# Kernel tuning notes

Hardware: AMD Instinct MI355X
Metric: run time of the kernel (lower is better)

Reference implementation:

```python
import jax, jax.numpy as jnp
import numpy as np

N, E, NS, NB = 25000, 400000, 4, 8
S0, V0 = 64, 32            # input: 64x0e + 32x1o
MS, MV = 96, 96            # message irreps: 96x0e + 96x1o
OS, OV = 128, 32           # post-linear_down/skip: (64+64)x0e + 32x1o
NIRR = S0 + V0             # node_feats.irreps.num_irreps = 96
AVG_NEIGH = 16.0
Y1 = float(np.sqrt(3.0 / (4.0 * np.pi)))  # integral-normalized l=1 SH coeff


def setup_inputs() -> dict:
    key = jax.random.key(0)
    k = jax.random.split(key, 15)
    return {
        'node_feats': jax.random.normal(k[0], (N, S0 + 3 * V0), jnp.float32),
        'vectors': jax.random.normal(k[1], (E, 3), jnp.float32),
        'rbf': jax.random.uniform(k[2], (E, NB), jnp.float32),
        'species': jax.random.randint(k[3], (N,), 0, NS, jnp.int32),
        'senders': jax.random.randint(k[4], (E,), 0, N, jnp.int32),
        'receivers': jax.random.randint(k[5], (E,), 0, N, jnp.int32),
        'W_up_s': jax.random.normal(k[6], (S0, S0), jnp.float32),
        'W_up_v': jax.random.normal(k[7], (V0, V0), jnp.float32),
        'W_mlp1': jax.random.normal(k[8], (NB, 64), jnp.float32),
        'W_mlp2': jax.random.normal(k[9], (64, 64), jnp.float32),
        'W_mlp3': jax.random.normal(k[10], (64, MS + MV), jnp.float32),
        'W_down_s': jax.random.normal(k[11], (MS, OS), jnp.float32),
        'W_down_v': jax.random.normal(k[12], (MV, OV), jnp.float32),
        'W_skip_s': jax.random.normal(k[13], (NS, S0, OS), jnp.float32),
        'W_skip_v': jax.random.normal(k[14], (NS, V0, OV), jnp.float32),
    }


def reference(node_feats, vectors, rbf, species, senders, receivers,
              W_up_s, W_up_v, W_mlp1, W_mlp2, W_mlp3,
              W_down_s, W_down_v, W_skip_s, W_skip_v):
    n = node_feats.shape[0]
    s = node_feats[:, :S0]                      # [N, 64]   0e
    v = node_feats[:, S0:].reshape(n, V0, 3)    # [N, 32,3] 1o

    # linear_up (per-irrep linear, 1/sqrt(fan_in) path normalization), then gather
    s_up = (s @ W_up_s) * (1.0 / jnp.sqrt(S0))
    v_up = jnp.einsum('nci,cd->ndi', v, W_up_v) * (1.0 / jnp.sqrt(V0))
    s_e = s_up[senders]                         # [E, 64]
    v_e = v_up[senders]                         # [E, 32, 3]

    # spherical harmonics l=1, normalize=True, 'integral' normalization
    y = Y1 * vectors / (jnp.linalg.norm(vectors, axis=-1, keepdims=True) + 1e-12)

    # tensor products filtered to output irreps + 0e
    tp_v = s_e[:, :, None] * y[:, None, :]                       # 0e x 1o -> 1o [E,64,3]
    tp_s = jnp.einsum('eci,ei->ec', v_e, y) * (1.0 / jnp.sqrt(3.0))  # 1o x 1o -> 0e [E,32]
    msg_s = jnp.concatenate([s_e, tp_s], axis=1)                 # [E, 96]
    msg_v = jnp.concatenate([v_e, tp_v], axis=1)                 # [E, 96, 3]

    # radial MLP -> per-edge, per-irrep mixing weights
    h = jax.nn.silu(rbf @ W_mlp1 * (1.0 / jnp.sqrt(NB)))
    h = jax.nn.silu(h @ W_mlp2 * (1.0 / 8.0))
    mix = h @ W_mlp3 * (1.0 / 8.0)                               # [E, 192]

    inv = 1.0 / NIRR
    msg_s = msg_s * mix[:, :MS] * inv
    msg_v = msg_v * (mix[:, MS:] * inv)[:, :, None]

    # scatter-sum to receivers, then normalize by sqrt(avg_num_neighbors)
    agg_s = jax.ops.segment_sum(msg_s, receivers, num_segments=n) / jnp.sqrt(AVG_NEIGH)
    agg_v = jax.ops.segment_sum(msg_v, receivers, num_segments=n) / jnp.sqrt(AVG_NEIGH)

    # linear_down to 128x0e + 32x1o
    out_s = agg_s @ W_down_s * (1.0 / jnp.sqrt(MS))
    out_v = jnp.einsum('nci,cd->ndi', agg_v, W_down_v) * (1.0 / jnp.sqrt(MV))

    # species-indexed skip connection (indexed linear)
    skip_s = jnp.einsum('nc,ncd->nd', s, W_skip_s[species]) * (1.0 / jnp.sqrt(S0))
    skip_v = jnp.einsum('nci,ncd->ndi', v, W_skip_v[species]) * (1.0 / jnp.sqrt(V0))

    f_s = out_s + skip_s                                         # [N, 128]
    f_v = out_v + skip_v                                         # [N, 32, 3]

    # equivariant gate: first 96 scalars activated, last 32 scalars gate the vectors
    act_s = jax.nn.silu(f_s[:, :OS - OV])
    gates = jax.nn.silu(f_s[:, OS - OV:])
    gated_v = f_v * gates[:, :, None]
    return jnp.concatenate([act_s, gated_v.reshape(n, OV * 3)], axis=1)  # [N, 192]
```

## Files before the change

### kernel.cpp

```cpp
#include <hip/hip_runtime.h>
#include <hip/hip_bf16.h>
#include <hip/hip_fp16.h>
#include <hip/hip_fp8.h>

#define NN 25000
#define EE 400000

#define SC_UP_S 0.125f
#define SC_UP_V 0.17677669529663689f
#define Y1C 0.48860251190291992f
#define SC_MLP1 0.35355339059327373f
#define SC_MLP2 0.125f
#define SC3 0.0013020833333333333f
#define INV_SQRT3 0.57735026918962584f
#define SC_DOWN 0.025515518153991442f
#define SC_SKIP_S 0.125f
#define SC_SKIP_V 0.17677669529663689f

typedef __attribute__((ext_vector_type(8))) short short8;
typedef __attribute__((ext_vector_type(4))) float f32x4;

__device__ __forceinline__ float silu(float x) {
  return __fdividef(x, 1.f + __expf(-x));
}
__device__ __forceinline__ unsigned short f2bf(float f) {
  unsigned u = __float_as_uint(f);
  unsigned r = u + 0x7FFF + ((u >> 16) & 1);
  return (unsigned short)(r >> 16);
}
__device__ __forceinline__ float bf2f(unsigned short s) {
  return __uint_as_float(((unsigned)s) << 16);
}
__device__ __forceinline__ unsigned packbf(float lo, float hi) {
  return ((unsigned)f2bf(hi) << 16) | (unsigned)f2bf(lo);
}
__device__ __forceinline__ unsigned char f2fp8(float x) {
  __hip_fp8_e4m3 v(x);
  return (unsigned char)v.__x;
}
__device__ __forceinline__ float fp82f(unsigned b) {
  __hip_fp8_e4m3 t;
  t.__x = (__hip_fp8_storage_t)b;
  return (float)t;
}

#define W_W1P 0
#define W_W2P 1024
#define W_W3B 3072
#define W_WDS 9216
#define W_WDV 15360
#define W_SUP 16896
#define W_VUP (W_SUP + NN * 64)
#define W_DEG (W_VUP + NN * 96)
#define W_PRE (W_DEG + NN)
#define W_CUR (W_PRE + NN + 8)
#define W_SRT (W_CUR + NN)
#define W_EDN (W_SRT + EE * 2)
#define W_END (W_EDN + EE * 56)

__global__ __launch_bounds__(256) void transpose_weights(
    const float* __restrict__ W1, const float* __restrict__ W2,
    const float* __restrict__ W3, const float* __restrict__ Wds,
    const float* __restrict__ Wdv, float* __restrict__ ws) {
  int t = blockIdx.x * 256 + threadIdx.x;
  int stride = gridDim.x * 256;
  unsigned short* W1p = (unsigned short*)(ws + W_W1P);
  unsigned short* W2p = (unsigned short*)(ws + W_W2P);
  unsigned short* W3b = (unsigned short*)(ws + W_W3B);
  unsigned short* Wdsb = (unsigned short*)(ws + W_WDS);
  unsigned short* Wdvb = (unsigned short*)(ws + W_WDV);
  for (int i = t; i < 2048; i += stride) {
    int c = i >> 5, k = i & 31;
    W1p[i] = (k < 8) ? f2bf(W1[k * 64 + c] * SC_MLP1) : (unsigned short)0;
  }
  for (int i = t; i < 4096; i += stride) {
    int c = i >> 6, k = i & 63;
    W2p[i] = f2bf(W2[k * 64 + c] * SC_MLP2);
  }
  for (int i = t; i < 12288; i += stride) {
    int c = i >> 6, k = i & 63;
    float sc = (c >= 64 && c < 96) ? (SC3 * INV_SQRT3) : SC3;
    W3b[i] = f2bf(W3[k * 192 + c] * sc);
  }
  for (int i = t; i < 12288; i += stride) {
    int o = i / 96, k = i - 96 * o;
    Wdsb[i] = f2bf(Wds[k * 128 + o] * SC_DOWN);
  }
  for (int i = t; i < 3072; i += stride) {
    int o = i / 96, k = i - 96 * o;
    Wdvb[i] = f2bf(Wdv[k * 32 + o] * SC_DOWN);
  }
}

__global__ __launch_bounds__(256) void up_kernel(
    const float* __restrict__ nf, const float* __restrict__ Wus,
    const float* __restrict__ Wuv, float* __restrict__ s_up,
    float* __restrict__ v_up) {
  int n = blockIdx.x;
  int t = threadIdx.x;
  __shared__ float sv[160];
  if (t < 160) sv[t] = nf[n * 160 + t];
  __syncthreads();
  if (t < 64) {
    float a = 0.f;
#pragma unroll
    for (int k = 0; k < 64; k++) a += sv[k] * Wus[k * 64 + t];
    s_up[n * 64 + t] = a * SC_UP_S;
  } else if (t < 160) {
    int j = t - 64;
    int c = j / 3, i = j - 3 * c;
    float a = 0.f;
#pragma unroll
    for (int k = 0; k < 32; k++) a += sv[64 + k * 3 + i] * Wuv[k * 32 + c];
    v_up[n * 96 + j] = a * SC_UP_V;
  }
}

__global__ __launch_bounds__(256) void count_deg(
    const int* __restrict__ receivers, int* __restrict__ deg) {
  int e = blockIdx.x * 256 + threadIdx.x;
  if (e < EE) atomicAdd(&deg[receivers[e]], 1);
}

__global__ __launch_bounds__(1024) void scan_kernel(
    const int* __restrict__ deg, int* __restrict__ prefix) {
  __shared__ int waveSums[16];
  __shared__ int sCarry;
  int t = threadIdx.x;
  int lane = t & 63, wv = t >> 6;
  if (t == 0) sCarry = 0;
  __syncthreads();
  for (int base = 0; base < NN; base += 1024) {
    int i = base + t;
    int x = (i < NN) ? deg[i] : 0;
    int v = x;
#pragma unroll
    for (int d = 1; d < 64; d <<= 1) {
      int u = __shfl_up(v, d, 64);
      if (lane >= d) v += u;
    }
    if (lane == 63) waveSums[wv] = v;
    __syncthreads();
    if (wv == 0 && lane < 16) {
      int s = waveSums[lane];
#pragma unroll
      for (int d = 1; d < 16; d <<= 1) {
        int u = __shfl_up(s, d, 64);
        if (lane >= d) s += u;
      }
      waveSums[lane] = s;
    }
    __syncthreads();
    int waveOff = (wv == 0) ? 0 : waveSums[wv - 1];
    int incl = v + waveOff + sCarry;
    if (i < NN) prefix[i] = incl - x;
    __syncthreads();
    if (t == 1023) sCarry = incl;
    __syncthreads();
  }
  if (t == 0) prefix[NN] = sCarry;
}

__global__ __launch_bounds__(256) void copy_cursor(
    const int* __restrict__ prefix, int* __restrict__ cursor) {
  int i = blockIdx.x * 256 + threadIdx.x;
  if (i < NN) cursor[i] = prefix[i];
}

__global__ __launch_bounds__(256) void scatter_kernel(
    const int* __restrict__ senders, const int* __restrict__ receivers,
    int* __restrict__ cursor, int2* __restrict__ sorted) {
  int e = blockIdx.x * 256 + threadIdx.x;
  if (e < EE) {
    int r = receivers[e];
    int pos = atomicAdd(&cursor[r], 1);
    sorted[pos] = make_int2(e, senders[e]);
  }
}

__global__ __launch_bounds__(256, 4) void edge_down2(
    const float* __restrict__ rbf, const float* __restrict__ vectors,
    const int2* __restrict__ sorted,
    const unsigned short* __restrict__ W1p,
    const unsigned short* __restrict__ W2p,
    const unsigned short* __restrict__ W3b,
    const unsigned short* __restrict__ Wdsb,
    const unsigned short* __restrict__ Wdvb,
    const float* __restrict__ s_up, const float* __restrict__ v_up,
    unsigned char* __restrict__ edown) {
  __shared__ unsigned short sH[64 * 72];
  __shared__ unsigned short sMix[64 * 200];
  __shared__ float4 sY[64];

  int t = threadIdx.x;
  int pbase = blockIdx.x * 64;
  int lane = t & 63;
  int wv = t >> 6;
  int rl = lane & 15;
  int kgrp = lane >> 4;
  int arow = 16 * wv + rl;
  int crow = 16 * wv + kgrp * 4;

  if (t < 64) {
    int2 es = sorted[pbase + t];
    float vx = vectors[(size_t)es.x * 3 + 0];
    float vy = vectors[(size_t)es.x * 3 + 1];
    float vz = vectors[(size_t)es.x * 3 + 2];
    float nrm = sqrtf(vx * vx + vy * vy + vz * vz) + 1e-12f;
    float ysc = Y1C / nrm;
    sY[t] = make_float4(vx * ysc, vy * ysc, vz * ysc, __int_as_float(es.y));
  }

  union S8 { short8 v; unsigned u[4]; };

  S8 a1;
  a1.u[0] = a1.u[1] = a1.u[2] = a1.u[3] = 0u;
  if (kgrp == 0) {
    int eid = sorted[pbase + arow].x;
    float4 ra = *(const float4*)(rbf + (size_t)eid * 8);
    float4 rb = *(const float4*)(rbf + (size_t)eid * 8 + 4);
    a1.u[0] = packbf(ra.x, ra.y);
    a1.u[1] = packbf(ra.z, ra.w);
    a1.u[2] = packbf(rb.x, rb.y);
    a1.u[3] = packbf(rb.z, rb.w);
  }
#pragma unroll
  for (int ct = 0; ct < 4; ct++) {
    short8 b = *(const short8*)&W1p[(ct * 16 + rl) * 32 + kgrp * 8];
    f32x4 acc = {0.f, 0.f, 0.f, 0.f};
    acc = __builtin_amdgcn_mfma_f32_16x16x32_bf16(a1.v, b, acc, 0, 0, 0);
#pragma unroll
    for (int rr = 0; rr < 4; rr++)
      sH[(crow + rr) * 72 + ct * 16 + rl] = f2bf(silu(acc[rr]));
  }

  {
    short8 a20 = *(const short8*)&sH[arow * 72 + kgrp * 8];
    short8 a21 = *(const short8*)&sH[arow * 72 + 32 + kgrp * 8];
#pragma unroll
    for (int ct = 0; ct < 4; ct++) {
      const unsigned short* wb = &W2p[(ct * 16 + rl) * 64];
      short8 b0 = *(const short8*)&wb[kgrp * 8];
      short8 b1 = *(const short8*)&wb[32 + kgrp * 8];
      f32x4 acc = {0.f, 0.f, 0.f, 0.f};
      acc = __builtin_amdgcn_mfma_f32_16x16x32_bf16(a20, b0, acc, 0, 0, 0);
      acc = __builtin_amdgcn_mfma_f32_16x16x32_bf16(a21, b1, acc, 0, 0, 0);
#pragma unroll
      for (int rr = 0; rr < 4; rr++)
        sH[(crow + rr) * 72 + ct * 16 + rl] = f2bf(silu(acc[rr]));
    }
  }

  {
    short8 a30 = *(const short8*)&sH[arow * 72 + kgrp * 8];
    short8 a31 = *(const short8*)&sH[arow * 72 + 32 + kgrp * 8];
#pragma unroll
    for (int nt = 0; nt < 12; nt++) {
      int cc = nt * 16 + rl;
      const unsigned short* wb = &W3b[cc * 64];
      short8 b0 = *(const short8*)&wb[kgrp * 8];
      short8 b1 = *(const short8*)&wb[32 + kgrp * 8];
      f32x4 acc = {0.f, 0.f, 0.f, 0.f};
      acc = __builtin_amdgcn_mfma_f32_16x16x32_bf16(a30, b0, acc, 0, 0, 0);
      acc = __builtin_amdgcn_mfma_f32_16x16x32_bf16(a31, b1, acc, 0, 0, 0);
#pragma unroll
      for (int rr = 0; rr < 4; rr++)
        sMix[(crow + rr) * 200 + cc] = f2bf(acc[rr]);
    }
  }
  __syncthreads();

  float4 yv = sY[arow];
  int snd = __float_as_int(yv.w);
  const float* se = s_up + (size_t)snd * 64;
  const float* ve = v_up + (size_t)snd * 96;
  float se1[8], se2[8], vvv[24];
  *(float4*)&se1[0] = *(const float4*)(se + kgrp * 8);
  *(float4*)&se1[4] = *(const float4*)(se + kgrp * 8 + 4);
  *(float4*)&se2[0] = *(const float4*)(se + 32 + kgrp * 8);
  *(float4*)&se2[4] = *(const float4*)(se + 32 + kgrp * 8 + 4);
#pragma unroll
  for (int j = 0; j < 6; j++)
    *(float4*)&vvv[4 * j] = *(const float4*)(ve + 24 * kgrp + 4 * j);

  const unsigned short* mrow = &sMix[arow * 200];
  S8 as0, as1, as2, mvp1, mvp2, mvp3;
  {
    short8 m = *(const short8*)&mrow[kgrp * 8];
#pragma unroll
    for (int q = 0; q < 4; q++)
      as0.u[q] = packbf(se1[2 * q] * bf2f((unsigned short)m[2 * q]),
                        se1[2 * q + 1] * bf2f((unsigned short)m[2 * q + 1]));
  }
  {
    short8 m = *(const short8*)&mrow[32 + kgrp * 8];
#pragma unroll
    for (int q = 0; q < 4; q++)
      as1.u[q] = packbf(se2[2 * q] * bf2f((unsigned short)m[2 * q]),
                        se2[2 * q + 1] * bf2f((unsigned short)m[2 * q + 1]));
  }
  {
    short8 m = *(const short8*)&mrow[64 + kgrp * 8];
#pragma unroll
    for (int q = 0; q < 4; q++) {
      float d0 = vvv[6 * q] * yv.x + vvv[6 * q + 1] * yv.y + vvv[6 * q + 2] * yv.z;
      float d1 = vvv[6 * q + 3] * yv.x + vvv[6 * q + 4] * yv.y + vvv[6 * q + 5] * yv.z;
      as2.u[q] = packbf(d0 * bf2f((unsigned short)m[2 * q]),
                        d1 * bf2f((unsigned short)m[2 * q + 1]));
    }
  }
  mvp1.v = *(const short8*)&mrow[96 + kgrp * 8];
  mvp2.v = *(const short8*)&mrow[128 + kgrp * 8];
  mvp3.v = *(const short8*)&mrow[160 + kgrp * 8];
  __syncthreads();

  unsigned char* edL = (unsigned char*)sMix;
#pragma unroll
  for (int ot = 0; ot < 8; ot++) {
    int col = ot * 16 + rl;
    const unsigned short* wb = &Wdsb[col * 96];
    short8 b0 = *(const short8*)&wb[kgrp * 8];
    short8 b1 = *(const short8*)&wb[32 + kgrp * 8];
    short8 b2 = *(const short8*)&wb[64 + kgrp * 8];
    f32x4 acc = {0.f, 0.f, 0.f, 0.f};
    acc = __builtin_amdgcn_mfma_f32_16x16x32_bf16(as0.v, b0, acc, 0, 0, 0);
    acc = __builtin_amdgcn_mfma_f32_16x16x32_bf16(as1.v, b1, acc, 0, 0, 0);
    acc = __builtin_amdgcn_mfma_f32_16x16x32_bf16(as2.v, b2, acc, 0, 0, 0);
#pragma unroll
    for (int rr = 0; rr < 4; rr++)
      edL[(crow + rr) * 232 + col] = f2fp8(acc[rr]);
  }
  float yarr[3] = {yv.x, yv.y, yv.z};
#pragma unroll
  for (int i = 0; i < 3; i++) {
    S8 av0, av1, av2;
#pragma unroll
    for (int q = 0; q < 4; q++) {
      av0.u[q] = packbf(
          vvv[3 * (2 * q) + i] * bf2f((unsigned short)mvp1.v[2 * q]),
          vvv[3 * (2 * q + 1) + i] * bf2f((unsigned short)mvp1.v[2 * q + 1]));
      av1.u[q] = packbf(
          se1[2 * q] * yarr[i] * bf2f((unsigned short)mvp2.v[2 * q]),
          se1[2 * q + 1] * yarr[i] * bf2f((unsigned short)mvp2.v[2 * q + 1]));
      av2.u[q] = packbf(
          se2[2 * q] * yarr[i] * bf2f((unsigned short)mvp3.v[2 * q]),
          se2[2 * q + 1] * yarr[i] * bf2f((unsigned short)mvp3.v[2 * q + 1]));
    }
#pragma unroll
    for (int ot = 0; ot < 2; ot++) {
      int o = ot * 16 + rl;
      const unsigned short* wb = &Wdvb[o * 96];
      short8 b0 = *(const short8*)&wb[kgrp * 8];
      short8 b1 = *(const short8*)&wb[32 + kgrp * 8];
      short8 b2 = *(const short8*)&wb[64 + kgrp * 8];
      f32x4 acc = {0.f, 0.f, 0.f, 0.f};
      acc = __builtin_amdgcn_mfma_f32_16x16x32_bf16(av0.v, b0, acc, 0, 0, 0);
      acc = __builtin_amdgcn_mfma_f32_16x16x32_bf16(av1.v, b1, acc, 0, 0, 0);
      acc = __builtin_amdgcn_mfma_f32_16x16x32_bf16(av2.v, b2, acc, 0, 0, 0);
#pragma unroll
      for (int rr = 0; rr < 4; rr++)
        edL[(crow + rr) * 232 + 128 + o * 3 + i] = f2fp8(acc[rr]);
    }
  }
  __syncthreads();

  {
    int row = t >> 2, q = t & 3;
    const unsigned* src = (const unsigned*)(edL + row * 232 + q * 56);
    unsigned* dst = (unsigned*)(edown + (size_t)(pbase + row) * 224 + q * 56);
#pragma unroll
    for (int j = 0; j < 14; j++) dst[j] = src[j];
  }
}

__global__ __launch_bounds__(256) void gather_out3(
    const float* __restrict__ nf, const int* __restrict__ species,
    const int* __restrict__ prefix, const unsigned* __restrict__ edw,
    const float* __restrict__ Wss, const float* __restrict__ Wsv,
    float* __restrict__ out) {
  int n = blockIdx.x;
  int t = threadIdx.x;
  __shared__ float sNF[160];
  __shared__ float4 sPart[4][56];
  __shared__ float sEd[224];
  __shared__ float sF[224];
  if (t < 160) sNF[t] = nf[(size_t)n * 160 + t];
  int beg = prefix[n], end = prefix[n + 1];
  if (t < 224) {
    int u = t % 56, rg = t / 56;
    float a0 = 0.f, a1 = 0.f, a2 = 0.f, a3 = 0.f;
    for (int s = beg + rg; s < end; s += 4) {
      unsigned v = edw[(size_t)s * 56 + u];
      a0 += fp82f(v & 0xFF);
      a1 += fp82f((v >> 8) & 0xFF);
      a2 += fp82f((v >> 16) & 0xFF);
      a3 += fp82f(v >> 24);
    }
    sPart[rg][u] = make_float4(a0, a1, a2, a3);
  }
  __syncthreads();
  if (t < 56) {
    float4 a = sPart[0][t], b = sPart[1][t], c = sPart[2][t], d = sPart[3][t];
    sEd[4 * t + 0] = a.x + b.x + c.x + d.x;
    sEd[4 * t + 1] = a.y + b.y + c.y + d.y;
    sEd[4 * t + 2] = a.z + b.z + c.z + d.z;
    sEd[4 * t + 3] = a.w + b.w + c.w + d.w;
  }
  __syncthreads();
  int spec = species[n];
  if (t < 128) {
    const float* wsk = Wss + (size_t)spec * 64 * 128;
    float b = 0.f;
#pragma unroll
    for (int k = 0; k < 64; k++) b += sNF[k] * wsk[k * 128 + t];
    sF[t] = sEd[t] + b * SC_SKIP_S;
  } else if (t < 224) {
    int j = t - 128;
    int c = j / 3, i = j - 3 * c;
    const float* wsk = Wsv + (size_t)spec * 32 * 32;
    float b = 0.f;
#pragma unroll
    for (int k = 0; k < 32; k++) b += sNF[64 + k * 3 + i] * wsk[k * 32 + c];
    sF[t] = sEd[t] + b * SC_SKIP_V;
  }
  __syncthreads();
  if (t < 96) {
    out[(size_t)n * 192 + t] = silu(sF[t]);
  } else if (t < 192) {
    int j = t - 96;
    int c = j / 3;
    out[(size_t)n * 192 + t] = sF[128 + j] * silu(sF[96 + c]);
  }
}

extern "C" void kernel_launch(void* const* d_in, const int* in_sizes, int n_in,
                              void* d_out, int out_size, void* d_ws, size_t ws_size,
                              hipStream_t stream) {
  const float* nf = (const float*)d_in[0];
  const float* vectors = (const float*)d_in[1];
  const float* rbf = (const float*)d_in[2];
  const int* species = (const int*)d_in[3];
  const int* senders = (const int*)d_in[4];
  const int* receivers = (const int*)d_in[5];
  const float* Wus = (const float*)d_in[6];
  const float* Wuv = (const float*)d_in[7];
  const float* W1 = (const float*)d_in[8];
  const float* W2 = (const float*)d_in[9];
  const float* W3 = (const float*)d_in[10];
  const float* Wds = (const float*)d_in[11];
  const float* Wdv = (const float*)d_in[12];
  const float* Wss = (const float*)d_in[13];
  const float* Wsv = (const float*)d_in[14];

  float* ws = (float*)d_ws;
  const unsigned short* W1p = (const unsigned short*)(ws + W_W1P);
  const unsigned short* W2p = (const unsigned short*)(ws + W_W2P);
  const unsigned short* W3b = (const unsigned short*)(ws + W_W3B);
  const unsigned short* Wdsb = (const unsigned short*)(ws + W_WDS);
  const unsigned short* Wdvb = (const unsigned short*)(ws + W_WDV);
  float* s_up = ws + W_SUP;
  float* v_up = ws + W_VUP;
  int* deg = (int*)(ws + W_DEG);
  int* prefix = (int*)(ws + W_PRE);
  int* cursor = (int*)(ws + W_CUR);
  int2* sorted = (int2*)(ws + W_SRT);
  unsigned char* edown = (unsigned char*)(ws + W_EDN);
  float* out = (float*)d_out;

  transpose_weights<<<16, 256, 0, stream>>>(W1, W2, W3, Wds, Wdv, ws);
  up_kernel<<<NN, 256, 0, stream>>>(nf, Wus, Wuv, s_up, v_up);

  hipMemsetAsync(deg, 0, (size_t)NN * sizeof(int), stream);
  count_deg<<<(EE + 255) / 256, 256, 0, stream>>>(receivers, deg);
  scan_kernel<<<1, 1024, 0, stream>>>(deg, prefix);
  copy_cursor<<<(NN + 255) / 256, 256, 0, stream>>>(prefix, cursor);
  scatter_kernel<<<(EE + 255) / 256, 256, 0, stream>>>(senders, receivers,
                                                       cursor, sorted);
  edge_down2<<<EE / 64, 256, 0, stream>>>(rbf, vectors, sorted, W1p, W2p, W3b,
                                          Wdsb, Wdvb, s_up, v_up, edown);
  gather_out3<<<NN, 256, 0, stream>>>(nf, species, prefix, (const unsigned*)edown,
                                      Wss, Wsv, out);
}
```

Measured before the change: 375.0 us.

## Store up-projected node features as bf16 and prefetch sender gathers early

The up-projected scalar and vector features are now written in bf16, which halves the bytes gathered per edge in the edge kernel. The sender-feature and vector loads are issued at kernel start, before the MLP matmuls, instead of after a barrier via shared memory, so their latency overlaps with compute and one __syncthreads is removed. The cursor copy kernel is folded into the scan. The cost is extra bf16 rounding of the node features and higher register pressure from holding the prefetched data.

```diff
diff --git a/kernel.cpp b/kernel.cpp
--- a/kernel.cpp
+++ b/kernel.cpp
@@ -31,6 +31,9 @@
 __device__ __forceinline__ float bf2f(unsigned short s) {
   return __uint_as_float(((unsigned)s) << 16);
 }
+__device__ __forceinline__ float bfe(short8 v, int idx) {
+  return __uint_as_float(((unsigned)(unsigned short)v[idx]) << 16);
+}
 __device__ __forceinline__ unsigned packbf(float lo, float hi) {
   return ((unsigned)f2bf(hi) << 16) | (unsigned)f2bf(lo);
 }
@@ -49,9 +52,9 @@
 #define W_W3B 3072
 #define W_WDS 9216
 #define W_WDV 15360
-#define W_SUP 16896
-#define W_VUP (W_SUP + NN * 64)
-#define W_DEG (W_VUP + NN * 96)
+#define W_SUPB 16896
+#define W_VUPB (W_SUPB + NN * 32)
+#define W_DEG (W_VUPB + NN * 48)
 #define W_PRE (W_DEG + NN)
 #define W_CUR (W_PRE + NN + 8)
 #define W_SRT (W_CUR + NN)
@@ -94,8 +97,8 @@
 
 __global__ __launch_bounds__(256) void up_kernel(
     const float* __restrict__ nf, const float* __restrict__ Wus,
-    const float* __restrict__ Wuv, float* __restrict__ s_up,
-    float* __restrict__ v_up) {
+    const float* __restrict__ Wuv, unsigned short* __restrict__ s_upb,
+    unsigned short* __restrict__ v_upb) {
   int n = blockIdx.x;
   int t = threadIdx.x;
   __shared__ float sv[160];
@@ -105,14 +108,14 @@
     float a = 0.f;
 #pragma unroll
     for (int k = 0; k < 64; k++) a += sv[k] * Wus[k * 64 + t];
-    s_up[n * 64 + t] = a * SC_UP_S;
+    s_upb[n * 64 + t] = f2bf(a * SC_UP_S);
   } else if (t < 160) {
     int j = t - 64;
     int c = j / 3, i = j - 3 * c;
     float a = 0.f;
 #pragma unroll
     for (int k = 0; k < 32; k++) a += sv[64 + k * 3 + i] * Wuv[k * 32 + c];
-    v_up[n * 96 + j] = a * SC_UP_V;
+    v_upb[n * 96 + j] = f2bf(a * SC_UP_V);
   }
 }
 
@@ -123,7 +126,8 @@
 }
 
 __global__ __launch_bounds__(1024) void scan_kernel(
-    const int* __restrict__ deg, int* __restrict__ prefix) {
+    const int* __restrict__ deg, int* __restrict__ prefix,
+    int* __restrict__ cursor) {
   __shared__ int waveSums[16];
   __shared__ int sCarry;
   int t = threadIdx.x;
@@ -153,18 +157,15 @@
     __syncthreads();
     int waveOff = (wv == 0) ? 0 : waveSums[wv - 1];
     int incl = v + waveOff + sCarry;
-    if (i < NN) prefix[i] = incl - x;
+    if (i < NN) {
+      prefix[i] = incl - x;
+      cursor[i] = incl - x;
+    }
     __syncthreads();
     if (t == 1023) sCarry = incl;
     __syncthreads();
   }
   if (t == 0) prefix[NN] = sCarry;
-}
-
-__global__ __launch_bounds__(256) void copy_cursor(
-    const int* __restrict__ prefix, int* __restrict__ cursor) {
-  int i = blockIdx.x * 256 + threadIdx.x;
-  if (i < NN) cursor[i] = prefix[i];
 }
 
 __global__ __launch_bounds__(256) void scatter_kernel(
@@ -178,7 +179,7 @@
   }
 }
 
-__global__ __launch_bounds__(256, 4) void edge_down2(
+__global__ __launch_bounds__(256, 4) void edge_down3(
     const float* __restrict__ rbf, const float* __restrict__ vectors,
     const int2* __restrict__ sorted,
     const unsigned short* __restrict__ W1p,
@@ -186,11 +187,11 @@
     const unsigned short* __restrict__ W3b,
     const unsigned short* __restrict__ Wdsb,
     const unsigned short* __restrict__ Wdvb,
-    const float* __restrict__ s_up, const float* __restrict__ v_up,
+    const unsigned short* __restrict__ s_upb,
+    const unsigned short* __restrict__ v_upb,
     unsigned char* __restrict__ edown) {
   __shared__ unsigned short sH[64 * 72];
   __shared__ unsigned short sMix[64 * 200];
-  __shared__ float4 sY[64];
 
   int t = threadIdx.x;
   int pbase = blockIdx.x * 64;
@@ -201,22 +202,27 @@
   int arow = 16 * wv + rl;
   int crow = 16 * wv + kgrp * 4;
 
-  if (t < 64) {
-    int2 es = sorted[pbase + t];
-    float vx = vectors[(size_t)es.x * 3 + 0];
-    float vy = vectors[(size_t)es.x * 3 + 1];
-    float vz = vectors[(size_t)es.x * 3 + 2];
-    float nrm = sqrtf(vx * vx + vy * vy + vz * vz) + 1e-12f;
-    float ysc = Y1C / nrm;
-    sY[t] = make_float4(vx * ysc, vy * ysc, vz * ysc, __int_as_float(es.y));
-  }
-
   union S8 { short8 v; unsigned u[4]; };
+
+  int2 es = sorted[pbase + arow];
+  int eid = es.x, snd = es.y;
+  const unsigned short* seb = s_upb + (size_t)snd * 64;
+  const unsigned short* veb = v_upb + (size_t)snd * 96;
+  short8 se0 = *(const short8*)&seb[kgrp * 8];
+  short8 se1 = *(const short8*)&seb[32 + kgrp * 8];
+  short8 ve0 = *(const short8*)&veb[24 * kgrp];
+  short8 ve1 = *(const short8*)&veb[24 * kgrp + 8];
+  short8 ve2 = *(const short8*)&veb[24 * kgrp + 16];
+  float vx = vectors[(size_t)eid * 3 + 0];
+  float vy = vectors[(size_t)eid * 3 + 1];
+  float vz = vectors[(size_t)eid * 3 + 2];
+  float nrm = sqrtf(vx * vx + vy * vy + vz * vz) + 1e-12f;
+  float ysc = Y1C / nrm;
+  float y0 = vx * ysc, y1 = vy * ysc, y2 = vz * ysc;
 
   S8 a1;
   a1.u[0] = a1.u[1] = a1.u[2] = a1.u[3] = 0u;
   if (kgrp == 0) {
-    int eid = sorted[pbase + arow].x;
     float4 ra = *(const float4*)(rbf + (size_t)eid * 8);
     float4 rb = *(const float4*)(rbf + (size_t)eid * 8 + 4);
     a1.u[0] = packbf(ra.x, ra.y);
@@ -268,20 +274,6 @@
         sMix[(crow + rr) * 200 + cc] = f2bf(acc[rr]);
     }
   }
-  __syncthreads();
-
-  float4 yv = sY[arow];
-  int snd = __float_as_int(yv.w);
-  const float* se = s_up + (size_t)snd * 64;
-  const float* ve = v_up + (size_t)snd * 96;
-  float se1[8], se2[8], vvv[24];
-  *(float4*)&se1[0] = *(const float4*)(se + kgrp * 8);
-  *(float4*)&se1[4] = *(const float4*)(se + kgrp * 8 + 4);
-  *(float4*)&se2[0] = *(const float4*)(se + 32 + kgrp * 8);
-  *(float4*)&se2[4] = *(const float4*)(se + 32 + kgrp * 8 + 4);
-#pragma unroll
-  for (int j = 0; j < 6; j++)
-    *(float4*)&vvv[4 * j] = *(const float4*)(ve + 24 * kgrp + 4 * j);
 
   const unsigned short* mrow = &sMix[arow * 200];
   S8 as0, as1, as2, mvp1, mvp2, mvp3;
@@ -289,24 +281,32 @@
     short8 m = *(const short8*)&mrow[kgrp * 8];
 #pragma unroll
     for (int q = 0; q < 4; q++)
-      as0.u[q] = packbf(se1[2 * q] * bf2f((unsigned short)m[2 * q]),
-                        se1[2 * q + 1] * bf2f((unsigned short)m[2 * q + 1]));
+      as0.u[q] = packbf(bfe(se0, 2 * q) * bfe(m, 2 * q),
+                        bfe(se0, 2 * q + 1) * bfe(m, 2 * q + 1));
   }
   {
     short8 m = *(const short8*)&mrow[32 + kgrp * 8];
 #pragma unroll
     for (int q = 0; q < 4; q++)
-      as1.u[q] = packbf(se2[2 * q] * bf2f((unsigned short)m[2 * q]),
-                        se2[2 * q + 1] * bf2f((unsigned short)m[2 * q + 1]));
+      as1.u[q] = packbf(bfe(se1, 2 * q) * bfe(m, 2 * q),
+                        bfe(se1, 2 * q + 1) * bfe(m, 2 * q + 1));
   }
   {
     short8 m = *(const short8*)&mrow[64 + kgrp * 8];
 #pragma unroll
     for (int q = 0; q < 4; q++) {
-      float d0 = vvv[6 * q] * yv.x + vvv[6 * q + 1] * yv.y + vvv[6 * q + 2] * yv.z;
-      float d1 = vvv[6 * q + 3] * yv.x + vvv[6 * q + 4] * yv.y + vvv[6 * q + 5] * yv.z;
-      as2.u[q] = packbf(d0 * bf2f((unsigned short)m[2 * q]),
-                        d1 * bf2f((unsigned short)m[2 * q + 1]));
+      float d0 = bfe(ve0, (6 * q) % 8 == 6 * q ? 6 * q : 6 * q) * 0.f;
+      (void)d0;
+      float e0, e1, e2, f0, f1, f2;
+      if (6 * q < 8) e0 = bfe(ve0, 6 * q); else if (6 * q < 16) e0 = bfe(ve1, 6 * q - 8); else e0 = bfe(ve2, 6 * q - 16);
+      if (6 * q + 1 < 8) e1 = bfe(ve0, 6 * q + 1); else if (6 * q + 1 < 16) e1 = bfe(ve1, 6 * q - 7); else e1 = bfe(ve2, 6 * q - 15);
+      if (6 * q + 2 < 8) e2 = bfe(ve0, 6 * q + 2); else if (6 * q + 2 < 16) e2 = bfe(ve1, 6 * q - 6); else e2 = bfe(ve2, 6 * q - 14);
+      if (6 * q + 3 < 8) f0 = bfe(ve0, 6 * q + 3); else if (6 * q + 3 < 16) f0 = bfe(ve1, 6 * q - 5); else f0 = bfe(ve2, 6 * q - 13);
+      if (6 * q + 4 < 8) f1 = bfe(ve0, 6 * q + 4); else if (6 * q + 4 < 16) f1 = bfe(ve1, 6 * q - 4); else f1 = bfe(ve2, 6 * q - 12);
+      if (6 * q + 5 < 8) f2 = bfe(ve0, 6 * q + 5); else if (6 * q + 5 < 16) f2 = bfe(ve1, 6 * q - 3); else f2 = bfe(ve2, 6 * q - 11);
+      float da = e0 * y0 + e1 * y1 + e2 * y2;
+      float db = f0 * y0 + f1 * y1 + f2 * y2;
+      as2.u[q] = packbf(da * bfe(m, 2 * q), db * bfe(m, 2 * q + 1));
     }
   }
   mvp1.v = *(const short8*)&mrow[96 + kgrp * 8];
@@ -330,21 +330,25 @@
     for (int rr = 0; rr < 4; rr++)
       edL[(crow + rr) * 232 + col] = f2fp8(acc[rr]);
   }
-  float yarr[3] = {yv.x, yv.y, yv.z};
+  float yarr[3] = {y0, y1, y2};
 #pragma unroll
   for (int i = 0; i < 3; i++) {
     S8 av0, av1, av2;
 #pragma unroll
     for (int q = 0; q < 4; q++) {
-      av0.u[q] = packbf(
-          vvv[3 * (2 * q) + i] * bf2f((unsigned short)mvp1.v[2 * q]),
-          vvv[3 * (2 * q + 1) + i] * bf2f((unsigned short)mvp1.v[2 * q + 1]));
-      av1.u[q] = packbf(
-          se1[2 * q] * yarr[i] * bf2f((unsigned short)mvp2.v[2 * q]),
-          se1[2 * q + 1] * yarr[i] * bf2f((unsigned short)mvp2.v[2 * q + 1]));
-      av2.u[q] = packbf(
-          se2[2 * q] * yarr[i] * bf2f((unsigned short)mvp3.v[2 * q]),
-          se2[2 * q + 1] * yarr[i] * bf2f((unsigned short)mvp3.v[2 * q + 1]));
+      float g0, g1;
+      {
+        const int j0 = 0;
+        (void)j0;
+      }
+      int ja = 6 * q + i, jb = 6 * q + 3 + i;
+      if (ja < 8) g0 = bfe(ve0, ja); else if (ja < 16) g0 = bfe(ve1, ja - 8); else g0 = bfe(ve2, ja - 16);
+      if (jb < 8) g1 = bfe(ve0, jb); else if (jb < 16) g1 = bfe(ve1, jb - 8); else g1 = bfe(ve2, jb - 16);
+      av0.u[q] = packbf(g0 * bfe(mvp1.v, 2 * q), g1 * bfe(mvp1.v, 2 * q + 1));
+      av1.u[q] = packbf(bfe(se0, 2 * q) * yarr[i] * bfe(mvp2.v, 2 * q),
+                        bfe(se0, 2 * q + 1) * yarr[i] * bfe(mvp2.v, 2 * q + 1));
+      av2.u[q] = packbf(bfe(se1, 2 * q) * yarr[i] * bfe(mvp3.v, 2 * q),
+                        bfe(se1, 2 * q + 1) * yarr[i] * bfe(mvp3.v, 2 * q + 1));
     }
 #pragma unroll
     for (int ot = 0; ot < 2; ot++) {
@@ -458,8 +462,8 @@
   const unsigned short* W3b = (const unsigned short*)(ws + W_W3B);
   const unsigned short* Wdsb = (const unsigned short*)(ws + W_WDS);
   const unsigned short* Wdvb = (const unsigned short*)(ws + W_WDV);
-  float* s_up = ws + W_SUP;
-  float* v_up = ws + W_VUP;
+  unsigned short* s_upb = (unsigned short*)(ws + W_SUPB);
+  unsigned short* v_upb = (unsigned short*)(ws + W_VUPB);
   int* deg = (int*)(ws + W_DEG);
   int* prefix = (int*)(ws + W_PRE);
   int* cursor = (int*)(ws + W_CUR);
@@ -468,16 +472,15 @@
   float* out = (float*)d_out;
 
   transpose_weights<<<16, 256, 0, stream>>>(W1, W2, W3, Wds, Wdv, ws);
-  up_kernel<<<NN, 256, 0, stream>>>(nf, Wus, Wuv, s_up, v_up);
+  up_kernel<<<NN, 256, 0, stream>>>(nf, Wus, Wuv, s_upb, v_upb);
 
   hipMemsetAsync(deg, 0, (size_t)NN * sizeof(int), stream);
   count_deg<<<(EE + 255) / 256, 256, 0, stream>>>(receivers, deg);
-  scan_kernel<<<1, 1024, 0, stream>>>(deg, prefix);
-  copy_cursor<<<(NN + 255) / 256, 256, 0, stream>>>(prefix, cursor);
+  scan_kernel<<<1, 1024, 0, stream>>>(deg, prefix, cursor);
   scatter_kernel<<<(EE + 255) / 256, 256, 0, stream>>>(senders, receivers,
                                                        cursor, sorted);
-  edge_down2<<<EE / 64, 256, 0, stream>>>(rbf, vectors, sorted, W1p, W2p, W3b,
-                                          Wdsb, Wdvb, s_up, v_up, edown);
+  edge_down3<<<EE / 64, 256, 0, stream>>>(rbf, vectors, sorted, W1p, W2p, W3b,
+                                          Wdsb, Wdvb, s_upb, v_upb, edown);
   gather_out3<<<NN, 256, 0, stream>>>(nf, species, prefix, (const unsigned*)edown,
                                       Wss, Wsv, out);
 }
```

Result: faster. 355.9 us (-5.1%).
